# Performance work log

Hardware: AMD Instinct MI355X
Metric: run time of the kernel (lower is better)

Reference implementation:

```python
import jax, jax.numpy as jnp
import numpy as np

LN_EPS = 1e-5
SUM_CLAMP = 1e-12


def setup_inputs() -> dict:
    key = jax.random.key(0)
    ks = jax.random.split(key, 10)
    L, D, H, P, E = 200000, 512, 512, 16384, 200000
    lesion_x = jax.random.normal(ks[0], (L, D), dtype=jnp.float32)
    edge_index = jnp.stack([
        jax.random.randint(ks[1], (E,), 0, P),   # patient idx
        jax.random.randint(ks[2], (E,), 0, L),   # lesion idx
    ], axis=0).astype(jnp.int64)
    s1 = 1.0 / np.sqrt(D)
    s2 = 1.0 / np.sqrt(H)
    W1 = jax.random.uniform(ks[3], (H, D), jnp.float32, -s1, s1)
    b1 = jax.random.uniform(ks[4], (H,), jnp.float32, -s1, s1)
    W2 = jax.random.uniform(ks[5], (1, H), jnp.float32, -s2, s2)
    b2 = jax.random.uniform(ks[6], (1,), jnp.float32, -s2, s2)
    Wp = jax.random.uniform(ks[7], (768, D), jnp.float32, -s1, s1)
    bp = jax.random.uniform(ks[8], (768,), jnp.float32, -s1, s1)
    gamma = jnp.ones((768,), jnp.float32)
    beta = jnp.zeros((768,), jnp.float32)
    return dict(lesion_x=lesion_x, patient_to_lesion_edge_index=edge_index,
                num_patients_in_batch=P, W1=W1, b1=b1, W2=W2, b2=b2,
                Wp=Wp, bp=bp, gamma=gamma, beta=beta)


def reference(lesion_x, patient_to_lesion_edge_index, num_patients_in_batch,
              W1, b1, W2, b2, Wp, bp, gamma, beta):
    P = int(num_patients_in_batch)
    pat = patient_to_lesion_edge_index[0]
    les = patient_to_lesion_edge_index[1]
    feats = lesion_x[les]                                  # [E, D] gather
    h = jnp.tanh(feats @ W1.T + b1)                        # [E, H]
    scores = (h @ W2.T + b2)[:, 0]                         # [E]
    smax = jax.ops.segment_max(scores, pat, num_segments=P)  # [P]
    ex = jnp.exp(scores - smax[pat])                       # [E]
    esum = jax.ops.segment_sum(ex, pat, num_segments=P)
    esum = jnp.maximum(esum, SUM_CLAMP)
    alpha = ex / esum[pat]                                 # [E]
    agg = jax.ops.segment_sum(feats * alpha[:, None], pat, num_segments=P)  # [P, D]
    proj = agg @ Wp.T + bp                                 # [P, 768]
    mu = jnp.mean(proj, axis=-1, keepdims=True)
    var = jnp.mean(jnp.square(proj - mu), axis=-1, keepdims=True)
    out = (proj - mu) * jax.lax.rsqrt(var + LN_EPS) * gamma + beta
    return out
```

## Files before the change

kernel.cpp:

```cpp
#include <hip/hip_runtime.h>
#include <hip/hip_bf16.h>

#define D_DIM 512
#define H_DIM 512
#define O_DIM 768

using bf16x8 = __attribute__((ext_vector_type(8))) short;
using f32x4  = __attribute__((ext_vector_type(4))) float;

static __device__ __forceinline__ unsigned short f2bf(float f){
  unsigned u = __float_as_uint(f);
  u += 0x7fffu + ((u >> 16) & 1u);
  return (unsigned short)(u >> 16);
}

static __device__ __forceinline__ unsigned cvtpk(float lo, float hi){
  unsigned r;
  asm("v_cvt_pk_bf16_f32 %0, %1, %2" : "=v"(r) : "v"(lo), "v"(hi));
  return r;
}

static __device__ __forceinline__ float fast_tanh(float x){
  float e = __expf(2.f * x);
  return 1.f - 2.f / (e + 1.f);
}

static __device__ __forceinline__ unsigned f2ord(float f){
  unsigned u = __float_as_uint(f);
  return (u & 0x80000000u) ? ~u : (u | 0x80000000u);
}
static __device__ __forceinline__ float ord2f(unsigned u){
  u = (u & 0x80000000u) ? (u & 0x7fffffffu) : ~u;
  return __uint_as_float(u);
}

static __device__ __forceinline__ void gload16(const void* g, void* l){
  __builtin_amdgcn_global_load_lds(
      (const __attribute__((address_space(1))) void*)g,
      (__attribute__((address_space(3))) void*)l, 16, 0, 0);
}

__global__ void cvt_bf16(const float* __restrict__ in,
                         unsigned short* __restrict__ out, int n8)
{
  int stride = gridDim.x * blockDim.x;
  for (int i = blockIdx.x*blockDim.x + threadIdx.x; i < n8; i += stride){
    const float4* p = (const float4*)in + (size_t)i*2;
    float4 a = p[0], b = p[1];
    union { unsigned short us[8]; uint4 u4; } pk;
    pk.us[0]=f2bf(a.x); pk.us[1]=f2bf(a.y); pk.us[2]=f2bf(a.z); pk.us[3]=f2bf(a.w);
    pk.us[4]=f2bf(b.x); pk.us[5]=f2bf(b.y); pk.us[6]=f2bf(b.z); pk.us[7]=f2bf(b.w);
    ((uint4*)out)[i] = pk.u4;
  }
}

__launch_bounds__(256, 2)
__global__ void gemm1_f32a(const float* __restrict__ A,
                           const short* __restrict__ Bm,
                           const float* __restrict__ bias,
                           const float* __restrict__ w2,
                           float* __restrict__ out,
                           int M, int nwg)
{
  __shared__ float lds_af[128*64];
  __shared__ short lds_b [128*64];

  {
  }
  const int q  = nwg >> 3, rr = nwg & 7;
  const int xcd = blockIdx.x & 7, bidx = blockIdx.x >> 3;
  const int swz = (xcd < rr ? xcd*(q+1) : rr*(q+1) + (xcd-rr)*q) + bidx;
  const int colBase = (swz & 3) * 128;
  const int rowBase = (swz >> 2) * 128;

  const int tid  = threadIdx.x;
  const int lane = tid & 63;
  const int w    = tid >> 6;
  const int wr   = w >> 1, wc = w & 1;
  const int lr   = lane & 15;
  const int lk   = lane >> 4;

  f32x4 acc[4][4];
  #pragma unroll
  for (int i = 0; i < 4; ++i)
    #pragma unroll
    for (int j = 0; j < 4; ++j)
      acc[i][j] = (f32x4){0.f, 0.f, 0.f, 0.f};

  const int rlocA = lane >> 4;
  const int jA    = lane & 15;
  const int rlocB = lane >> 3;
  const int jB    = lane & 7;

  for (int kt = 0; kt < 512/64; ++kt){
    const int kOff = kt * 64;
    #pragma unroll
    for (int c = 0; c < 8; ++c){
      int rt = w*32 + c*4 + rlocA;
      int gA = rowBase + rt; if (gA > M-1) gA = M-1;
      int js = jA ^ (rt & 7);
      gload16(A + (size_t)gA*512 + kOff + js*4, &lds_af[(w*32 + c*4)*64]);
    }
    #pragma unroll
    for (int c = 0; c < 4; ++c){
      int rt = w*32 + c*8 + rlocB;
      int gB = colBase + rt;
      int js = jB ^ (rt & 7);
      gload16(Bm + (size_t)gB*512 + kOff + js*8, &lds_b[(w*32 + c*8)*64]);
    }
    __syncthreads();
    #pragma unroll
    for (int kk = 0; kk < 2; ++kk){
      bf16x8 af[4], bfr[4];
      #pragma unroll
      for (int mf = 0; mf < 4; ++mf){
        int r   = wr*64 + mf*16 + lr;
        int rx  = r & 7;
        int g0  = kk*8 + lk*2;
        float4 lo4 = *(const float4*)&lds_af[r*64 + ((g0     ^ rx) << 2)];
        float4 hi4 = *(const float4*)&lds_af[r*64 + (((g0+1) ^ rx) << 2)];
        union { bf16x8 v; unsigned u[4]; } fa;
        fa.u[0] = cvtpk(lo4.x, lo4.y);
        fa.u[1] = cvtpk(lo4.z, lo4.w);
        fa.u[2] = cvtpk(hi4.x, hi4.y);
        fa.u[3] = cvtpk(hi4.z, hi4.w);
        af[mf] = fa.v;
      }
      #pragma unroll
      for (int nf = 0; nf < 4; ++nf){
        int r   = wc*64 + nf*16 + lr;
        int idx = (r*64 + kk*32 + lk*8) ^ ((r & 7) << 3);
        bfr[nf] = *(bf16x8*)&lds_b[idx];
      }
      #pragma unroll
      for (int mf = 0; mf < 4; ++mf)
        #pragma unroll
        for (int nf = 0; nf < 4; ++nf)
          acc[mf][nf] = __builtin_amdgcn_mfma_f32_16x16x32_bf16(
              af[mf], bfr[nf], acc[mf][nf], 0, 0, 0);
    }
    __syncthreads();
  }

  #pragma unroll
  for (int mf = 0; mf < 4; ++mf){
    float part[4] = {0.f,0.f,0.f,0.f};
    #pragma unroll
    for (int nf = 0; nf < 4; ++nf){
      int gc = colBase + wc*64 + nf*16 + lr;
      float b = bias[gc], wv = w2[gc];
      #pragma unroll
      for (int r = 0; r < 4; ++r)
        part[r] += fast_tanh(acc[mf][nf][r] + b) * wv;
    }
    #pragma unroll
    for (int r = 0; r < 4; ++r){
      part[r] += __shfl_xor(part[r], 1);
      part[r] += __shfl_xor(part[r], 2);
      part[r] += __shfl_xor(part[r], 4);
      part[r] += __shfl_xor(part[r], 8);
    }
    if (lr == 0){
      int gr = rowBase + wr*64 + mf*16 + lk*4;
      #pragma unroll
      for (int r = 0; r < 4; ++r)
        if (gr + r < M) atomicAdd(&out[gr + r], part[r]);
    }
  }
}

__launch_bounds__(256, 2)
__global__ void gemm2_bf16(const short* __restrict__ A,
                           const short* __restrict__ Bm,
                           const float* __restrict__ bias,
                           float* __restrict__ out,
                           int M, int outStride)
{
  __shared__ short lds_a[128*64];
  __shared__ short lds_b[128*64];

  const int tid  = threadIdx.x;
  const int lane = tid & 63;
  const int w    = tid >> 6;
  const int wr   = w >> 1, wc = w & 1;
  const int lr   = lane & 15;
  const int lk   = lane >> 4;

  const int colBase = blockIdx.x * 128;
  const int rowBase = blockIdx.y * 128;

  f32x4 acc[4][4];
  #pragma unroll
  for (int i = 0; i < 4; ++i)
    #pragma unroll
    for (int j = 0; j < 4; ++j)
      acc[i][j] = (f32x4){0.f, 0.f, 0.f, 0.f};

  const int subrow = lane >> 3;
  const int gpre   = lane & 7;

  for (int kt = 0; kt < 512/64; ++kt){
    const int kOff = kt * 64;
    #pragma unroll
    for (int c = 0; c < 4; ++c){
      int r    = w*32 + c*8 + subrow;
      int gran = gpre ^ (r & 7);
      int gA   = rowBase + r; if (gA > M-1) gA = M-1;
      gload16(A  + (size_t)gA*512 + kOff + gran*8, &lds_a[(w*32 + c*8)*64]);
      int gB   = colBase + r;
      gload16(Bm + (size_t)gB*512 + kOff + gran*8, &lds_b[(w*32 + c*8)*64]);
    }
    __syncthreads();
    #pragma unroll
    for (int kk = 0; kk < 2; ++kk){
      bf16x8 af[4], bfr[4];
      #pragma unroll
      for (int mf = 0; mf < 4; ++mf){
        int r   = wr*64 + mf*16 + lr;
        int idx = (r*64 + kk*32 + lk*8) ^ ((r & 7) << 3);
        af[mf] = *(bf16x8*)&lds_a[idx];
      }
      #pragma unroll
      for (int nf = 0; nf < 4; ++nf){
        int r   = wc*64 + nf*16 + lr;
        int idx = (r*64 + kk*32 + lk*8) ^ ((r & 7) << 3);
        bfr[nf] = *(bf16x8*)&lds_b[idx];
      }
      #pragma unroll
      for (int mf = 0; mf < 4; ++mf)
        #pragma unroll
        for (int nf = 0; nf < 4; ++nf)
          acc[mf][nf] = __builtin_amdgcn_mfma_f32_16x16x32_bf16(
              af[mf], bfr[nf], acc[mf][nf], 0, 0, 0);
    }
    __syncthreads();
  }

  #pragma unroll
  for (int mf = 0; mf < 4; ++mf){
    int gr = rowBase + wr*64 + mf*16 + lk*4;
    #pragma unroll
    for (int nf = 0; nf < 4; ++nf){
      int gc = colBase + wc*64 + nf*16 + lr;
      float b = bias[gc];
      #pragma unroll
      for (int r = 0; r < 4; ++r)
        if (gr + r < M) out[(size_t)(gr + r)*outStride + gc] = acc[mf][nf][r] + b;
    }
  }
}

__global__ void edge_pass1(const int* __restrict__ edge, int E,
                           const float* __restrict__ scores,
                           unsigned* __restrict__ smax_o,
                           int* __restrict__ hist)
{
  int e = blockIdx.x*256 + threadIdx.x;
  if (e >= E) return;
  int p = edge[e], l = edge[E + e];
  atomicMax(&smax_o[p], f2ord(scores[l]));
  atomicAdd(&hist[p], 1);
}

__global__ void scan_kernel(const int* __restrict__ hist,
                            int* __restrict__ offsets, int P)
{
  __shared__ int s[1024];
  int t = threadIdx.x;
  int local[16]; int sum = 0;
  #pragma unroll
  for (int i = 0; i < 16; ++i){
    int idx = t*16 + i;
    local[i] = (idx < P) ? hist[idx] : 0;
    sum += local[i];
  }
  s[t] = sum;
  __syncthreads();
  for (int off = 1; off < 1024; off <<= 1){
    int v = (t >= off) ? s[t - off] : 0;
    __syncthreads();
    s[t] += v;
    __syncthreads();
  }
  int run = s[t] - sum;
  #pragma unroll
  for (int i = 0; i < 16; ++i){
    int idx = t*16 + i;
    if (idx < P) offsets[idx] = run;
    run += local[i];
  }
}

__global__ void edge_pass2(const int* __restrict__ edge, int E,
                           const float* __restrict__ scores,
                           const unsigned* __restrict__ smax_o,
                           float* __restrict__ ex,
                           float* __restrict__ esum,
                           const int* __restrict__ offsets,
                           int* __restrict__ cursor,
                           int* __restrict__ sorted)
{
  int e = blockIdx.x*256 + threadIdx.x;
  if (e >= E) return;
  int p = edge[e], l = edge[E + e];
  float v = __expf(scores[l] - ord2f(smax_o[p]));
  ex[e] = v;
  atomicAdd(&esum[p], v);
  int pos = atomicAdd(&cursor[p], 1);
  sorted[offsets[p] + pos] = e;
}

__global__ void agg_kernel(const int* __restrict__ edge, int E,
                           const float* __restrict__ lesion_x,
                           const float* __restrict__ ex,
                           const float* __restrict__ esum,
                           const int* __restrict__ offsets,
                           const int* __restrict__ hist,
                           const int* __restrict__ sorted,
                           unsigned* __restrict__ aggb)
{
  int p = blockIdx.x;
  int n = hist[p];
  if (n == 0) return;
  int start = offsets[p];
  float inv = 1.f / fmaxf(esum[p], 1e-12f);
  int t = threadIdx.x;
  float a0 = 0.f, a1 = 0.f;
  for (int i = 0; i < n; ++i){
    int e = sorted[start + i];
    int l = edge[E + e];
    float alpha = ex[e] * inv;
    float2 f = *(const float2*)(lesion_x + (size_t)l*512 + t*2);
    a0 += alpha * f.x;
    a1 += alpha * f.y;
  }
  aggb[(size_t)p*256 + t] = cvtpk(a0, a1);
}

__global__ void ln_kernel(float* __restrict__ out,
                          const float* __restrict__ gamma,
                          const float* __restrict__ beta)
{
  __shared__ float red1[4];
  __shared__ float red2[4];
  int p = blockIdx.x;
  float* row = out + (size_t)p*768;
  int t = threadIdx.x;
  float v0 = row[t], v1 = row[t+256], v2 = row[t+512];
  float s = v0 + v1 + v2;
  #pragma unroll
  for (int off = 32; off; off >>= 1) s += __shfl_down(s, off);
  int lane = t & 63, wv = t >> 6;
  if (lane == 0) red1[wv] = s;
  __syncthreads();
  float mean = (red1[0]+red1[1]+red1[2]+red1[3]) * (1.f/768.f);
  float d0 = v0-mean, d1 = v1-mean, d2 = v2-mean;
  float q = d0*d0 + d1*d1 + d2*d2;
  #pragma unroll
  for (int off = 32; off; off >>= 1) q += __shfl_down(q, off);
  if (lane == 0) red2[wv] = q;
  __syncthreads();
  float var = (red2[0]+red2[1]+red2[2]+red2[3]) * (1.f/768.f);
  float inv = rsqrtf(var + 1e-5f);
  row[t]     = d0*inv*gamma[t]     + beta[t];
  row[t+256] = d1*inv*gamma[t+256] + beta[t+256];
  row[t+512] = d2*inv*gamma[t+512] + beta[t+512];
}

extern "C" void kernel_launch(void* const* d_in, const int* in_sizes, int n_in,
                              void* d_out, int out_size, void* d_ws, size_t ws_size,
                              hipStream_t stream)
{
  const float* lesion_x = (const float*)d_in[0];
  const int*   edge     = (const int*)d_in[1];
  const float* W1    = (const float*)d_in[3];
  const float* b1    = (const float*)d_in[4];
  const float* W2    = (const float*)d_in[5];
  const float* Wp    = (const float*)d_in[7];
  const float* bp    = (const float*)d_in[8];
  const float* gamma = (const float*)d_in[9];
  const float* beta  = (const float*)d_in[10];

  const int L = in_sizes[0] / D_DIM;
  const int E = in_sizes[1] / 2;
  const int P = out_size / O_DIM;

  auto al = [](size_t x){ return (x + 255) & ~(size_t)255; };
  char* ws = (char*)d_ws;
  size_t oScores = 0;
  size_t oSmax   = oScores + al((size_t)L*4);
  size_t oEsum   = oSmax   + al((size_t)P*4);
  size_t oHist   = oEsum   + al((size_t)P*4);
  size_t oCursor = oHist   + al((size_t)P*4);
  size_t smallEnd= oCursor + al((size_t)P*4);
  size_t oAggB   = smallEnd;
  size_t aggEnd  = oAggB   + al((size_t)P*D_DIM*2);
  size_t oOff    = aggEnd;
  size_t oEx     = oOff    + al((size_t)P*4);
  size_t oSorted = oEx     + al((size_t)E*4);
  size_t oW1b    = oSorted + al((size_t)E*4);
  size_t oWpb    = oW1b    + al((size_t)H_DIM*D_DIM*2);
  size_t need    = oWpb    + al((size_t)O_DIM*D_DIM*2);
  (void)need;

  float*    scores = (float*)(ws + oScores);
  unsigned* smax_o = (unsigned*)(ws + oSmax);
  float*    esum   = (float*)(ws + oEsum);
  int*      hist   = (int*)(ws + oHist);
  int*      cursor = (int*)(ws + oCursor);
  unsigned* aggb   = (unsigned*)(ws + oAggB);
  int*      offs   = (int*)(ws + oOff);
  float*    ex     = (float*)(ws + oEx);
  int*      sorted = (int*)(ws + oSorted);
  short*    W1b    = (short*)(ws + oW1b);
  short*    Wpb    = (short*)(ws + oWpb);

  hipMemsetAsync(d_ws, 0, smallEnd, stream);
  hipMemsetAsync(ws + oAggB, 0, (size_t)P*D_DIM*2, stream);

  dim3 b256(256);
  int eb = (E + 255) / 256;

  cvt_bf16<<<128, b256, 0, stream>>>(W1, (unsigned short*)W1b, H_DIM*D_DIM/8);
  cvt_bf16<<<192, b256, 0, stream>>>(Wp, (unsigned short*)Wpb, O_DIM*D_DIM/8);

  int nRow = (L + 127) / 128;
  int nwg  = 4 * nRow;
  gemm1_f32a<<<nwg, b256, 0, stream>>>(lesion_x, W1b, b1, W2, scores, L, nwg);

  edge_pass1<<<eb, b256, 0, stream>>>(edge, E, scores, smax_o, hist);
  scan_kernel<<<1, 1024, 0, stream>>>(hist, offs, P);
  edge_pass2<<<eb, b256, 0, stream>>>(edge, E, scores, smax_o, ex, esum,
                                      offs, cursor, sorted);
  agg_kernel<<<P, b256, 0, stream>>>(edge, E, lesion_x, ex, esum, offs,
                                     hist, sorted, aggb);
  gemm2_bf16<<<dim3(O_DIM/128, P/128), b256, 0, stream>>>(
      (const short*)aggb, Wpb, bp, (float*)d_out, P, O_DIM);
  ln_kernel<<<P, b256, 0, stream>>>((float*)d_out, gamma, beta);
}
```

Measured before the change: 430.0 us.

## Convert lesion rows to bf16 in registers before LDS and reuse them in aggregation

The first GEMM now loads fp32 lesion rows through registers, converts them to bf16 once, and stores bf16 into LDS. The old path kept fp32 tiles in LDS and converted at every fragment read. Blocks in the first column tile also write a bf16 copy of lesion_x to workspace. The aggregation kernel then gathers that half-size bf16 copy, with one wavefront per patient and 16-byte loads. This cuts LDS footprint (occupancy hint raised to 3) and gather bandwidth, at the cost of an extra global write of the bf16 matrix, register-staged loads instead of direct-to-LDS loads, and bf16 rounding of features in the aggregation.

```diff
diff --git a/kernel.cpp b/kernel.cpp
--- a/kernel.cpp
+++ b/kernel.cpp
@@ -20,6 +20,13 @@
   return r;
 }
 
+static __device__ __forceinline__ float bflo(unsigned u){
+  return __uint_as_float(u << 16);
+}
+static __device__ __forceinline__ float bfhi(unsigned u){
+  return __uint_as_float(u & 0xffff0000u);
+}
+
 static __device__ __forceinline__ float fast_tanh(float x){
   float e = __expf(2.f * x);
   return 1.f - 2.f / (e + 1.f);
@@ -47,31 +54,33 @@
   for (int i = blockIdx.x*blockDim.x + threadIdx.x; i < n8; i += stride){
     const float4* p = (const float4*)in + (size_t)i*2;
     float4 a = p[0], b = p[1];
-    union { unsigned short us[8]; uint4 u4; } pk;
-    pk.us[0]=f2bf(a.x); pk.us[1]=f2bf(a.y); pk.us[2]=f2bf(a.z); pk.us[3]=f2bf(a.w);
-    pk.us[4]=f2bf(b.x); pk.us[5]=f2bf(b.y); pk.us[6]=f2bf(b.z); pk.us[7]=f2bf(b.w);
-    ((uint4*)out)[i] = pk.u4;
-  }
-}
-
-__launch_bounds__(256, 2)
-__global__ void gemm1_f32a(const float* __restrict__ A,
-                           const short* __restrict__ Bm,
-                           const float* __restrict__ bias,
-                           const float* __restrict__ w2,
-                           float* __restrict__ out,
-                           int M, int nwg)
-{
-  __shared__ float lds_af[128*64];
-  __shared__ short lds_b [128*64];
-
-  {
-  }
+    uint4 pk = { cvtpk(a.x,a.y) | 0u, 0u, 0u, 0u };
+    pk.x = cvtpk(a.x, a.y);
+    pk.y = cvtpk(a.z, a.w);
+    pk.z = cvtpk(b.x, b.y);
+    pk.w = cvtpk(b.z, b.w);
+    ((uint4*)out)[i] = pk;
+  }
+}
+
+__launch_bounds__(256, 3)
+__global__ void gemm1_rs(const float* __restrict__ A,
+                         const short* __restrict__ Bm,
+                         const float* __restrict__ bias,
+                         const float* __restrict__ w2,
+                         float* __restrict__ out,
+                         short* __restrict__ Ab,
+                         int M, int nwg)
+{
+  __shared__ short lds_a[128*64];
+  __shared__ short lds_b[128*64];
+
   const int q  = nwg >> 3, rr = nwg & 7;
   const int xcd = blockIdx.x & 7, bidx = blockIdx.x >> 3;
   const int swz = (xcd < rr ? xcd*(q+1) : rr*(q+1) + (xcd-rr)*q) + bidx;
   const int colBase = (swz & 3) * 128;
   const int rowBase = (swz >> 2) * 128;
+  const bool writeAb = (colBase == 0);
 
   const int tid  = threadIdx.x;
   const int lane = tid & 63;
@@ -80,6 +89,11 @@
   const int lr   = lane & 15;
   const int lk   = lane >> 4;
 
+  const int srow = tid >> 4;
+  const int sgf  = tid & 15;
+  const int rlocB = lane >> 3;
+  const int jB    = lane & 7;
+
   f32x4 acc[4][4];
   #pragma unroll
   for (int i = 0; i < 4; ++i)
@@ -87,26 +101,31 @@
     for (int j = 0; j < 4; ++j)
       acc[i][j] = (f32x4){0.f, 0.f, 0.f, 0.f};
 
-  const int rlocA = lane >> 4;
-  const int jA    = lane & 15;
-  const int rlocB = lane >> 3;
-  const int jB    = lane & 7;
-
   for (int kt = 0; kt < 512/64; ++kt){
     const int kOff = kt * 64;
     #pragma unroll
-    for (int c = 0; c < 8; ++c){
-      int rt = w*32 + c*4 + rlocA;
-      int gA = rowBase + rt; if (gA > M-1) gA = M-1;
-      int js = jA ^ (rt & 7);
-      gload16(A + (size_t)gA*512 + kOff + js*4, &lds_af[(w*32 + c*4)*64]);
-    }
-    #pragma unroll
     for (int c = 0; c < 4; ++c){
       int rt = w*32 + c*8 + rlocB;
-      int gB = colBase + rt;
       int js = jB ^ (rt & 7);
-      gload16(Bm + (size_t)gB*512 + kOff + js*8, &lds_b[(w*32 + c*8)*64]);
+      gload16(Bm + (size_t)(colBase + rt)*512 + kOff + js*8,
+              &lds_b[(w*32 + c*8)*64]);
+    }
+    float4 va[8];
+    #pragma unroll
+    for (int c = 0; c < 8; ++c){
+      int gA = rowBase + c*16 + srow; if (gA > M-1) gA = M-1;
+      va[c] = *(const float4*)(A + (size_t)gA*512 + kOff + sgf*4);
+    }
+    #pragma unroll
+    for (int c = 0; c < 8; ++c){
+      int rt = c*16 + srow;
+      uint2 pk = { cvtpk(va[c].x, va[c].y), cvtpk(va[c].z, va[c].w) };
+      int sidx = (rt*64 + sgf*4) ^ ((rt & 7) << 3);
+      *(uint2*)&lds_a[sidx] = pk;
+      if (writeAb){
+        int gA = rowBase + rt;
+        if (gA < M) *(uint2*)(Ab + (size_t)gA*512 + kOff + sgf*4) = pk;
+      }
     }
     __syncthreads();
     #pragma unroll
@@ -115,16 +134,8 @@
       #pragma unroll
       for (int mf = 0; mf < 4; ++mf){
         int r   = wr*64 + mf*16 + lr;
-        int rx  = r & 7;
-        int g0  = kk*8 + lk*2;
-        float4 lo4 = *(const float4*)&lds_af[r*64 + ((g0     ^ rx) << 2)];
-        float4 hi4 = *(const float4*)&lds_af[r*64 + (((g0+1) ^ rx) << 2)];
-        union { bf16x8 v; unsigned u[4]; } fa;
-        fa.u[0] = cvtpk(lo4.x, lo4.y);
-        fa.u[1] = cvtpk(lo4.z, lo4.w);
-        fa.u[2] = cvtpk(hi4.x, hi4.y);
-        fa.u[3] = cvtpk(hi4.z, hi4.w);
-        af[mf] = fa.v;
+        int idx = (r*64 + kk*32 + lk*8) ^ ((r & 7) << 3);
+        af[mf] = *(bf16x8*)&lds_a[idx];
       }
       #pragma unroll
       for (int nf = 0; nf < 4; ++nf){
@@ -311,7 +322,7 @@
 }
 
 __global__ void agg_kernel(const int* __restrict__ edge, int E,
-                           const float* __restrict__ lesion_x,
+                           const short* __restrict__ Ab,
                            const float* __restrict__ ex,
                            const float* __restrict__ esum,
                            const int* __restrict__ offsets,
@@ -319,22 +330,26 @@
                            const int* __restrict__ sorted,
                            unsigned* __restrict__ aggb)
 {
-  int p = blockIdx.x;
+  int p    = blockIdx.x*4 + (threadIdx.x >> 6);
+  int lane = threadIdx.x & 63;
   int n = hist[p];
   if (n == 0) return;
   int start = offsets[p];
   float inv = 1.f / fmaxf(esum[p], 1e-12f);
-  int t = threadIdx.x;
-  float a0 = 0.f, a1 = 0.f;
+  float a[8] = {0.f,0.f,0.f,0.f,0.f,0.f,0.f,0.f};
   for (int i = 0; i < n; ++i){
     int e = sorted[start + i];
     int l = edge[E + e];
     float alpha = ex[e] * inv;
-    float2 f = *(const float2*)(lesion_x + (size_t)l*512 + t*2);
-    a0 += alpha * f.x;
-    a1 += alpha * f.y;
-  }
-  aggb[(size_t)p*256 + t] = cvtpk(a0, a1);
+    uint4 u = *(const uint4*)(Ab + (size_t)l*512 + lane*8);
+    a[0] += alpha * bflo(u.x);  a[1] += alpha * bfhi(u.x);
+    a[2] += alpha * bflo(u.y);  a[3] += alpha * bfhi(u.y);
+    a[4] += alpha * bflo(u.z);  a[5] += alpha * bfhi(u.z);
+    a[6] += alpha * bflo(u.w);  a[7] += alpha * bfhi(u.w);
+  }
+  uint4 o = { cvtpk(a[0],a[1]), cvtpk(a[2],a[3]),
+              cvtpk(a[4],a[5]), cvtpk(a[6],a[7]) };
+  *(uint4*)&aggb[(size_t)p*256 + lane*4] = o;
 }
 
 __global__ void ln_kernel(float* __restrict__ out,
@@ -355,10 +370,10 @@
   __syncthreads();
   float mean = (red1[0]+red1[1]+red1[2]+red1[3]) * (1.f/768.f);
   float d0 = v0-mean, d1 = v1-mean, d2 = v2-mean;
-  float q = d0*d0 + d1*d1 + d2*d2;
-  #pragma unroll
-  for (int off = 32; off; off >>= 1) q += __shfl_down(q, off);
-  if (lane == 0) red2[wv] = q;
+  float qq = d0*d0 + d1*d1 + d2*d2;
+  #pragma unroll
+  for (int off = 32; off; off >>= 1) qq += __shfl_down(qq, off);
+  if (lane == 0) red2[wv] = qq;
   __syncthreads();
   float var = (red2[0]+red2[1]+red2[2]+red2[3]) * (1.f/768.f);
   float inv = rsqrtf(var + 1e-5f);
@@ -400,7 +415,8 @@
   size_t oSorted = oEx     + al((size_t)E*4);
   size_t oW1b    = oSorted + al((size_t)E*4);
   size_t oWpb    = oW1b    + al((size_t)H_DIM*D_DIM*2);
-  size_t need    = oWpb    + al((size_t)O_DIM*D_DIM*2);
+  size_t oAb     = oWpb    + al((size_t)O_DIM*D_DIM*2);
+  size_t need    = oAb     + al((size_t)L*D_DIM*2);
   (void)need;
 
   float*    scores = (float*)(ws + oScores);
@@ -414,6 +430,7 @@
   int*      sorted = (int*)(ws + oSorted);
   short*    W1b    = (short*)(ws + oW1b);
   short*    Wpb    = (short*)(ws + oWpb);
+  short*    Ab     = (short*)(ws + oAb);
 
   hipMemsetAsync(d_ws, 0, smallEnd, stream);
   hipMemsetAsync(ws + oAggB, 0, (size_t)P*D_DIM*2, stream);
@@ -426,14 +443,14 @@
 
   int nRow = (L + 127) / 128;
   int nwg  = 4 * nRow;
-  gemm1_f32a<<<nwg, b256, 0, stream>>>(lesion_x, W1b, b1, W2, scores, L, nwg);
+  gemm1_rs<<<nwg, b256, 0, stream>>>(lesion_x, W1b, b1, W2, scores, Ab, L, nwg);
 
   edge_pass1<<<eb, b256, 0, stream>>>(edge, E, scores, smax_o, hist);
   scan_kernel<<<1, 1024, 0, stream>>>(hist, offs, P);
   edge_pass2<<<eb, b256, 0, stream>>>(edge, E, scores, smax_o, ex, esum,
                                       offs, cursor, sorted);
-  agg_kernel<<<P, b256, 0, stream>>>(edge, E, lesion_x, ex, esum, offs,
-                                     hist, sorted, aggb);
+  agg_kernel<<<P/4, b256, 0, stream>>>(edge, E, Ab, ex, esum, offs,
+                                       hist, sorted, aggb);
   gemm2_bf16<<<dim3(O_DIM/128, P/128), b256, 0, stream>>>(
       (const short*)aggb, Wpb, bp, (float*)d_out, P, O_DIM);
   ln_kernel<<<P, b256, 0, stream>>>((float*)d_out, gamma, beta);
```

After: 413.7 us. 3.8% less time.
